# Kernel optimization log

Measured on AMD Instinct MI355X. Metric: run time of the kernel, lower is better.

## Reference

```python
import jax, jax.numpy as jnp
import numpy as np

DELTA_VAR = 1.0
DELTA_DIST = 2.0
VAR_W = 1.0
DIST_W = 1.0
REG_W = 1.0


def _per_sample_loss(X, L, K, delta_reg):
    # X: [N, d] embeddings, L: [N] int cluster ids in [0, K)
    N, d = X.shape
    ind = (L[None, :] == jnp.arange(K)[:, None]).astype(X.dtype)  # [K, N]
    sizes = ind.sum(axis=1)                                       # [K]
    centers = (ind @ X) / sizes[:, None]                          # [K, d]
    # distance of each point to each cluster center: [K, N]
    dist = jnp.sqrt(((X[None, :, :] - centers[:, None, :]) ** 2).sum(axis=2))
    err = jnp.clip(dist - DELTA_VAR, 0.0) ** 2
    var_terms = (ind * err).sum(axis=1) / sizes                   # [K]
    var_term = var_terms.mean()
    # pairwise center distances: [K, K]
    dmat = jnp.sqrt(((centers[None, :, :] - centers[:, None, :]) ** 2).sum(axis=2))
    eye = jnp.eye(K, dtype=X.dtype)
    dist_cost = jnp.clip(DELTA_DIST - (dmat + eye * DELTA_DIST), 0.0) ** 2
    dist_term = dist_cost.sum() / (K * (K - 1))
    center_norms = jnp.sqrt((centers ** 2).sum(axis=1))
    reg_term = (jnp.clip(center_norms - delta_reg, 0.0) ** 2).mean()
    return var_term, dist_term, reg_term


def setup_inputs() -> dict:
    key = jax.random.key(0)
    k1, k2 = jax.random.split(key)
    B, d, H, W, K = 8, 16, 512, 512, 8
    data = jax.random.normal(k1, (B, d, H, W), dtype=jnp.float32)
    labels = jax.random.randint(k2, (B, H, W), 0, K, dtype=jnp.int64)
    return {"data": data, "labels": labels, "n_clusters": K}


def reference(data, labels, n_clusters):
    B, d, H, W = data.shape
    delta_reg = jnp.sqrt(jnp.asarray(d, dtype=data.dtype))
    X = data.reshape(B, d, H * W).transpose(0, 2, 1)  # [B, N, d]
    L = labels.reshape(B, H * W)                      # [B, N]
    var_t, dist_t, reg_t = jax.vmap(
        lambda x, l: _per_sample_loss(x, l, n_clusters, delta_reg)
    )(X, L)
    loss = VAR_W * var_t.mean() + DIST_W * dist_t.mean() + REG_W * reg_t.mean()
    return loss
```

## Files before the change

kernel.cpp:

```cpp
#include <hip/hip_runtime.h>
#include <hip/hip_bf16.h>

#define BB 8
#define DD 16
#define KK 8
#define NN (512 * 512)
#define G4 (NN / 4)

constexpr int BPB = 256;
constexpr int T   = 256;
constexpr int WV  = 4;
constexpr int WPB = BPB * WV;
constexpr int SL  = WPB * 8;
constexpr int IT1 = G4 / SL;

#define WS_SUMS    0
#define WS_CNTS    1024
#define WS_VARSUMS 1088
#define WS_TOTAL   1152

__global__ __launch_bounds__(T, 4) void k_sums(const float* __restrict__ data,
                                               const int* __restrict__ labels,
                                               float* __restrict__ ws) {
    const int b    = blockIdx.x / BPB;
    const int blk  = blockIdx.x % BPB;
    const int tid  = threadIdx.x;
    const int wv   = tid >> 6;
    const int lane = tid & 63;
    const int d8   = lane >> 3;
    const int r8   = lane & 7;
    const int w    = blk * WV + wv;

    const float4* dlo = (const float4*)(data + (size_t)b * DD * NN) + (size_t)d8 * G4;
    const float4* dhi = dlo + (size_t)8 * G4;
    const int4*   lp4 = (const int4*)(labels + (size_t)b * NN);

    float slo[KK], shi[KK];
    unsigned int cnt[KK];
#pragma unroll
    for (int k = 0; k < KK; ++k) { slo[k] = 0.f; shi[k] = 0.f; cnt[k] = 0u; }

#pragma unroll 4
    for (int i = 0; i < IT1; ++i) {
        const int gg = i * SL + w * 8 + r8;
        float4 xlo = dlo[gg];
        float4 xhi = dhi[gg];
        int4   lb  = lp4[gg];
        int   labs[4] = {lb.x, lb.y, lb.z, lb.w};
        float xl[4]   = {xlo.x, xlo.y, xlo.z, xlo.w};
        float xh[4]   = {xhi.x, xhi.y, xhi.z, xhi.w};
#pragma unroll
        for (int p = 0; p < 4; ++p) {
            const int   l = labs[p];
            const float a = xl[p];
            const float h = xh[p];
#pragma unroll
            for (int k = 0; k < KK; ++k) {
                bool m = (l == k);
                slo[k] += m ? a : 0.f;
                shi[k] += m ? h : 0.f;
                cnt[k] += (unsigned)__popcll(__ballot(m));
            }
        }
    }

#pragma unroll
    for (int k = 0; k < KK; ++k) {
#pragma unroll
        for (int m = 1; m < 8; m <<= 1) {
            slo[k] += __shfl_xor(slo[k], m, 64);
            shi[k] += __shfl_xor(shi[k], m, 64);
        }
    }

    __shared__ float sred[WV][DD][KK];
    __shared__ float cred[WV][KK];
    if (r8 == 0) {
#pragma unroll
        for (int k = 0; k < KK; ++k) {
            sred[wv][d8][k]     = slo[k];
            sred[wv][d8 + 8][k] = shi[k];
        }
    }
    if (lane == 0) {
#pragma unroll
        for (int k = 0; k < KK; ++k) cred[wv][k] = (float)(cnt[k] >> 3);
    }
    __syncthreads();

    if (tid < DD * KK) {
        const int dd = tid >> 3, k = tid & 7;
        float v = 0.f;
#pragma unroll
        for (int q = 0; q < WV; ++q) v += sred[q][dd][k];
        atomicAdd(&ws[WS_SUMS + (b * KK + k) * DD + dd], v);
    } else if (tid < DD * KK + KK) {
        const int k = tid - DD * KK;
        float v = 0.f;
#pragma unroll
        for (int q = 0; q < WV; ++q) v += cred[q][k];
        atomicAdd(&ws[WS_CNTS + b * KK + k], v);
    }
}

__global__ __launch_bounds__(T, 8) void k_var(const float* __restrict__ data,
                                              const int* __restrict__ labels,
                                              float* __restrict__ ws) {
    const int b   = blockIdx.x / BPB;
    const int blk = blockIdx.x % BPB;
    const int tid = threadIdx.x;

    __shared__ float cs[KK * 17 + DD];
    if (tid < KK * DD) {
        const int k = tid >> 4, d = tid & 15;
        cs[k * 17 + d] = ws[WS_SUMS + (b * KK + k) * DD + d] / ws[WS_CNTS + b * KK + k];
    }
    __syncthreads();

    const float4* dp4 = (const float4*)(data + (size_t)b * DD * NN);
    const int4*   lp4 = (const int4*)(labels + (size_t)b * NN);
    const int g = blk * T + tid;

    int4 lb = lp4[g];
    int labs[4] = {lb.x, lb.y, lb.z, lb.w};
    float ss[4] = {0.f, 0.f, 0.f, 0.f};
#pragma unroll 4
    for (int d = 0; d < DD; ++d) {
        float4 x = dp4[(size_t)d * G4 + g];
        float xs[4] = {x.x, x.y, x.z, x.w};
#pragma unroll
        for (int p = 0; p < 4; ++p) {
            float c  = cs[labs[p] * 17 + d];
            float df = xs[p] - c;
            ss[p] = fmaf(df, df, ss[p]);
        }
    }

    float acc[KK];
#pragma unroll
    for (int k = 0; k < KK; ++k) acc[k] = 0.f;
#pragma unroll
    for (int p = 0; p < 4; ++p) {
        float e  = fmaxf(sqrtf(ss[p]) - 1.0f, 0.f);
        float e2 = e * e;
#pragma unroll
        for (int k = 0; k < KK; ++k) acc[k] += (labs[p] == k) ? e2 : 0.f;
    }

    const int lane = tid & 63, wv = tid >> 6;
#pragma unroll
    for (int k = 0; k < KK; ++k) {
#pragma unroll
        for (int m = 1; m < 64; m <<= 1) acc[k] += __shfl_xor(acc[k], m, 64);
    }
    __shared__ float vred[WV][KK];
    if (lane == 0) {
#pragma unroll
        for (int k = 0; k < KK; ++k) vred[wv][k] = acc[k];
    }
    __syncthreads();
    if (tid < KK) {
        float v = 0.f;
#pragma unroll
        for (int q = 0; q < WV; ++q) v += vred[q][tid];
        atomicAdd(&ws[WS_VARSUMS + b * KK + tid], v);
    }
}

__global__ void k_final(const float* __restrict__ ws, float* __restrict__ out) {
    const int t = threadIdx.x;
    const int b = t >> 3, k = t & 7;
    const float inv = 1.0f / ws[WS_CNTS + t];
    __shared__ float sc[BB * KK][DD];
    float cen[DD];
    float n2 = 0.f;
#pragma unroll
    for (int d = 0; d < DD; ++d) {
        float v = ws[WS_SUMS + t * DD + d] * inv;
        cen[d] = v;
        sc[t][d] = v;
        n2 = fmaf(v, v, n2);
    }
    __syncthreads();
    float rg = fmaxf(sqrtf(n2) - 4.0f, 0.f);
    rg *= rg;
    float rowcost = 0.f;
#pragma unroll
    for (int j = 0; j < KK; ++j) {
        float d2 = 0.f;
#pragma unroll
        for (int d = 0; d < DD; ++d) {
            float df = cen[d] - sc[b * KK + j][d];
            d2 = fmaf(df, df, d2);
        }
        float dm = sqrtf(d2) + ((j == k) ? 2.0f : 0.0f);
        float h = fmaxf(2.0f - dm, 0.f);
        rowcost += h * h;
    }
    float var  = ws[WS_VARSUMS + t] * inv;
    float term = var / (float)KK + rowcost / 56.0f + rg / (float)KK;
#pragma unroll
    for (int m = 1; m < 64; m <<= 1) term += __shfl_xor(term, m, 64);
    if (t == 0) out[0] = term / (float)BB;
}

extern "C" void kernel_launch(void* const* d_in, const int* in_sizes, int n_in,
                              void* d_out, int out_size, void* d_ws, size_t ws_size,
                              hipStream_t stream) {
    const float* data   = (const float*)d_in[0];
    const int*   labels = (const int*)d_in[1];
    float*       ws     = (float*)d_ws;

    hipMemsetAsync(d_ws, 0, WS_TOTAL * sizeof(float), stream);
    k_sums<<<BB * BPB, T, 0, stream>>>(data, labels, ws);
    k_var<<<BB * BPB, T, 0, stream>>>(data, labels, ws);
    k_final<<<1, 64, 0, stream>>>(ws, (float*)d_out);
}
```

Baseline: 236.1 us.

## Split cluster-sum kernel per feature plane and drop per-element ballot counting

Each k_sums block now handles one (batch, feature, slab) triple and reads one contiguous feature plane plus the labels, instead of lanes splitting 8 feature pairs. Cluster counts are computed only by d==0 blocks using float accumulation, which removes the per-cluster ballot/popcount from the inner loop. Full-wave shuffles replace the 8-lane reduction, and occupancy hints rise. In exchange, labels are re-read once per feature plane, adding L2/cache traffic, and the d==0 blocks do extra work, which creates imbalance.

```diff
diff --git a/kernel.cpp b/kernel.cpp
--- a/kernel.cpp
+++ b/kernel.cpp
@@ -10,56 +10,55 @@
 constexpr int BPB = 256;
 constexpr int T   = 256;
 constexpr int WV  = 4;
-constexpr int WPB = BPB * WV;
-constexpr int SL  = WPB * 8;
-constexpr int IT1 = G4 / SL;
 
 #define WS_SUMS    0
 #define WS_CNTS    1024
 #define WS_VARSUMS 1088
 #define WS_TOTAL   1152
 
-__global__ __launch_bounds__(T, 4) void k_sums(const float* __restrict__ data,
+__global__ __launch_bounds__(T, 8) void k_sums(const float* __restrict__ data,
                                                const int* __restrict__ labels,
                                                float* __restrict__ ws) {
-    const int b    = blockIdx.x / BPB;
-    const int blk  = blockIdx.x % BPB;
+    const int e    = blockIdx.x;
+    const int b    = e & 7;
+    const int rem  = e >> 3;
+    const int d    = rem & 15;
+    const int sb   = rem >> 4;
     const int tid  = threadIdx.x;
     const int wv   = tid >> 6;
     const int lane = tid & 63;
-    const int d8   = lane >> 3;
-    const int r8   = lane & 7;
-    const int w    = blk * WV + wv;
-
-    const float4* dlo = (const float4*)(data + (size_t)b * DD * NN) + (size_t)d8 * G4;
-    const float4* dhi = dlo + (size_t)8 * G4;
+
+    const float4* dpl = (const float4*)(data + ((size_t)b * DD + d) * NN);
     const int4*   lp4 = (const int4*)(labels + (size_t)b * NN);
 
-    float slo[KK], shi[KK];
-    unsigned int cnt[KK];
-#pragma unroll
-    for (int k = 0; k < KK; ++k) { slo[k] = 0.f; shi[k] = 0.f; cnt[k] = 0u; }
+    const int gbase = sb * 4096 + wv * 1024 + lane;
+
+    float s[KK], c[KK];
+#pragma unroll
+    for (int k = 0; k < KK; ++k) { s[k] = 0.f; c[k] = 0.f; }
 
 #pragma unroll 4
-    for (int i = 0; i < IT1; ++i) {
-        const int gg = i * SL + w * 8 + r8;
-        float4 xlo = dlo[gg];
-        float4 xhi = dhi[gg];
-        int4   lb  = lp4[gg];
+    for (int i = 0; i < 16; ++i) {
+        const int g = gbase + i * 64;
+        float4 x  = dpl[g];
+        int4   lb = lp4[g];
         int   labs[4] = {lb.x, lb.y, lb.z, lb.w};
-        float xl[4]   = {xlo.x, xlo.y, xlo.z, xlo.w};
-        float xh[4]   = {xhi.x, xhi.y, xhi.z, xhi.w};
+        float xs[4]   = {x.x, x.y, x.z, x.w};
 #pragma unroll
         for (int p = 0; p < 4; ++p) {
             const int   l = labs[p];
-            const float a = xl[p];
-            const float h = xh[p];
-#pragma unroll
-            for (int k = 0; k < KK; ++k) {
-                bool m = (l == k);
-                slo[k] += m ? a : 0.f;
-                shi[k] += m ? h : 0.f;
-                cnt[k] += (unsigned)__popcll(__ballot(m));
+            const float a = xs[p];
+#pragma unroll
+            for (int k = 0; k < KK; ++k)
+                s[k] += (l == k) ? a : 0.f;
+        }
+        if (d == 0) {
+#pragma unroll
+            for (int p = 0; p < 4; ++p) {
+                const int l = labs[p];
+#pragma unroll
+                for (int k = 0; k < KK; ++k)
+                    c[k] += (l == k) ? 1.f : 0.f;
             }
         }
     }
@@ -67,38 +66,30 @@
 #pragma unroll
     for (int k = 0; k < KK; ++k) {
 #pragma unroll
-        for (int m = 1; m < 8; m <<= 1) {
-            slo[k] += __shfl_xor(slo[k], m, 64);
-            shi[k] += __shfl_xor(shi[k], m, 64);
-        }
-    }
-
-    __shared__ float sred[WV][DD][KK];
+        for (int m = 1; m < 64; m <<= 1) s[k] += __shfl_xor(s[k], m, 64);
+    }
+    if (d == 0) {
+#pragma unroll
+        for (int k = 0; k < KK; ++k) {
+#pragma unroll
+            for (int m = 1; m < 64; m <<= 1) c[k] += __shfl_xor(c[k], m, 64);
+        }
+    }
+
+    __shared__ float sred[WV][KK];
     __shared__ float cred[WV][KK];
-    if (r8 == 0) {
-#pragma unroll
-        for (int k = 0; k < KK; ++k) {
-            sred[wv][d8][k]     = slo[k];
-            sred[wv][d8 + 8][k] = shi[k];
-        }
-    }
     if (lane == 0) {
 #pragma unroll
-        for (int k = 0; k < KK; ++k) cred[wv][k] = (float)(cnt[k] >> 3);
-    }
-    __syncthreads();
-
-    if (tid < DD * KK) {
-        const int dd = tid >> 3, k = tid & 7;
-        float v = 0.f;
-#pragma unroll
-        for (int q = 0; q < WV; ++q) v += sred[q][dd][k];
-        atomicAdd(&ws[WS_SUMS + (b * KK + k) * DD + dd], v);
-    } else if (tid < DD * KK + KK) {
-        const int k = tid - DD * KK;
-        float v = 0.f;
-#pragma unroll
-        for (int q = 0; q < WV; ++q) v += cred[q][k];
+        for (int k = 0; k < KK; ++k) { sred[wv][k] = s[k]; cred[wv][k] = c[k]; }
+    }
+    __syncthreads();
+
+    if (tid < KK) {
+        float v = sred[0][tid] + sred[1][tid] + sred[2][tid] + sred[3][tid];
+        atomicAdd(&ws[WS_SUMS + (b * KK + tid) * DD + d], v);
+    } else if (d == 0 && tid >= 64 && tid < 64 + KK) {
+        const int k = tid - 64;
+        float v = cred[0][k] + cred[1][k] + cred[2][k] + cred[3][k];
         atomicAdd(&ws[WS_CNTS + b * KK + k], v);
     }
 }
@@ -212,7 +203,7 @@
     float*       ws     = (float*)d_ws;
 
     hipMemsetAsync(d_ws, 0, WS_TOTAL * sizeof(float), stream);
-    k_sums<<<BB * BPB, T, 0, stream>>>(data, labels, ws);
+    k_sums<<<2048, T, 0, stream>>>(data, labels, ws);
     k_var<<<BB * BPB, T, 0, stream>>>(data, labels, ws);
     k_final<<<1, 64, 0, stream>>>(ws, (float*)d_out);
 }
```

Result: no change. 239.0 us (+1.2%).
